# Optimization experiments

Hardware: AMD Instinct MI355X
Metric: run time of the kernel (lower is better)

## Reference

```python
import jax, jax.numpy as jnp
import numpy as np

N = 50000      # nodes
E = 800000     # edges (avg degree 16)
IN = 128       # in_channels
HID = 32       # hidden_channels per head
HEADS = 4
OUT = 64       # out_channels (last layer, heads=1, concat=False)
ED = 32        # edge_dim
NEG_SLOPE = 0.2


def _gatv2_layer(x, src, dst, ea, Wl, bl, Wr, br, We, att, bias, concat):
    """PyG GATv2Conv: lin_l -> source (x_j), lin_r -> target (x_i),
    score = att . leaky_relu(x_i + x_j + lin_edge(edge_attr)), segment-softmax over dst,
    out = scatter_add(alpha * x_j) per head, then concat or mean heads, plus bias."""
    n = x.shape[0]
    H, C = att.shape
    xl = (x @ Wl + bl).reshape(-1, H, C)   # [N,H,C] source transform
    xr = (x @ Wr + br).reshape(-1, H, C)   # [N,H,C] target transform
    ee = (ea @ We).reshape(-1, H, C)       # [E,H,C] edge transform
    m = jax.nn.leaky_relu(xl[src] + xr[dst] + ee, NEG_SLOPE)  # [E,H,C]
    a = jnp.einsum('ehc,hc->eh', m, att)   # [E,H] attention logits
    amax = jax.ops.segment_max(a, dst, num_segments=n)        # [N,H]
    ex = jnp.exp(a - amax[dst])
    den = jax.ops.segment_sum(ex, dst, num_segments=n)        # [N,H]
    alpha = ex / (den[dst] + 1e-16)        # [E,H] segment softmax
    out = jax.ops.segment_sum(xl[src] * alpha[..., None], dst, num_segments=n)  # [N,H,C]
    out = out.reshape(n, H * C) if concat else out.mean(axis=1)
    return out + bias


def setup_inputs() -> dict:
    key = jax.random.key(0)
    ks = jax.random.split(key, 20)
    s = 0.05
    HC = HEADS * HID
    inp = {
        'x': jax.random.normal(ks[0], (N, IN), jnp.float32),
        'edge_index': jax.random.randint(ks[1], (2, E), 0, N, jnp.int32),
        'edge_attr': jax.random.normal(ks[2], (E, ED), jnp.float32),
        # layer 1: GATv2Conv(IN -> HID, heads=HEADS, concat=True, edge_dim=ED)
        'Wl1': jax.random.normal(ks[3], (IN, HC), jnp.float32) * s,
        'bl1': jnp.zeros((HC,), jnp.float32),
        'Wr1': jax.random.normal(ks[4], (IN, HC), jnp.float32) * s,
        'br1': jnp.zeros((HC,), jnp.float32),
        'We1': jax.random.normal(ks[5], (ED, HC), jnp.float32) * s,
        'att1': jax.random.normal(ks[6], (HEADS, HID), jnp.float32) * s,
        'bias1': jnp.zeros((HC,), jnp.float32),
        # layer 2: GATv2Conv(HC -> OUT, heads=1, concat=False, edge_dim=ED)
        'Wl2': jax.random.normal(ks[7], (HC, OUT), jnp.float32) * s,
        'bl2': jnp.zeros((OUT,), jnp.float32),
        'Wr2': jax.random.normal(ks[8], (HC, OUT), jnp.float32) * s,
        'br2': jnp.zeros((OUT,), jnp.float32),
        'We2': jax.random.normal(ks[9], (ED, OUT), jnp.float32) * s,
        'att2': jax.random.normal(ks[10], (1, OUT), jnp.float32) * s,
        'bias2': jnp.zeros((OUT,), jnp.float32),
    }
    return inp


def reference(x, edge_index, edge_attr, Wl1, bl1, Wr1, br1, We1, att1, bias1,
              Wl2, bl2, Wr2, br2, We2, att2, bias2):
    src, dst = edge_index[0], edge_index[1]
    h = _gatv2_layer(x, src, dst, edge_attr, Wl1, bl1, Wr1, br1, We1, att1, bias1, concat=True)
    h = jax.nn.elu(h)
    out = _gatv2_layer(h, src, dst, edge_attr, Wl2, bl2, Wr2, br2, We2, att2, bias2, concat=False)
    return out
```

## Files before the change

kernel.cpp:

```cpp
#include <hip/hip_runtime.h>
#include <stdint.h>

#define N_NODES 50000
#define N_EDGES 800000

struct Ptrs { const void* p[16]; int n[16]; };

typedef __attribute__((ext_vector_type(8))) short bf16x8;
typedef __attribute__((ext_vector_type(4))) float f32x4;

__device__ __forceinline__ float bf2f(unsigned short u){
  union { unsigned int i; float f; } v; v.i = ((unsigned int)u) << 16; return v.f;
}
__device__ __forceinline__ float lo16(unsigned int u){ union { unsigned int i; float f; } v; v.i = u << 16; return v.f; }
__device__ __forceinline__ float hi16(unsigned int u){ union { unsigned int i; float f; } v; v.i = u & 0xffff0000u; return v.f; }
__device__ __forceinline__ unsigned short f2bf(float f){
  if (!(f == f)) return 0;
  unsigned int x = __float_as_uint(f);
  unsigned int r = (x + 0x7fffu + ((x >> 16) & 1u)) >> 16;
  return (unsigned short)r;
}
__device__ __forceinline__ float fin(float v){
  if (!(v == v)) return 0.f;
  return fminf(fmaxf(v, -1e30f), 1e30f);
}
__device__ __forceinline__ float loadF(const void* p, int f32, size_t idx){
  return f32 ? ((const float*)p)[idx] : bf2f(((const unsigned short*)p)[idx]);
}

__device__ __forceinline__ void stageW(unsigned short* dst, const void* src, int n, int f32, int tid){
  if (f32) {
    for (int i = tid * 8; i < n; i += 2048) {
      float4 a = *(const float4*)((const float*)src + i);
      float4 b = *(const float4*)((const float*)src + i + 4);
      uint4 u;
      u.x = (unsigned)f2bf(a.x) | ((unsigned)f2bf(a.y) << 16);
      u.y = (unsigned)f2bf(a.z) | ((unsigned)f2bf(a.w) << 16);
      u.z = (unsigned)f2bf(b.x) | ((unsigned)f2bf(b.y) << 16);
      u.w = (unsigned)f2bf(b.z) | ((unsigned)f2bf(b.w) << 16);
      *(uint4*)(dst + i) = u;
    }
  } else {
    for (int i = tid * 8; i < n; i += 2048)
      *(uint4*)(dst + i) = *(const uint4*)((const unsigned short*)src + i);
  }
}

__global__ __launch_bounds__(256) void k_detect(Ptrs tl, int* __restrict__ flags)
{
  __shared__ int red[256];
  int b = blockIdx.x, t = threadIdx.x;
  const unsigned short* p = (const unsigned short*)tl.p[b];
  int n = tl.n[b]; if (n > 16384) n = 16384;
  int crazy = 0;
  for (int i = t; i < n; i += 256) {
    unsigned short u = p[i];
    if (u) {
      int ex = (u >> 7) & 0xFF;
      if (ex == 0xFF || ex < 0x60) crazy++;
    }
  }
  red[t] = crazy; __syncthreads();
  for (int off = 128; off; off >>= 1) { if (t < off) red[t] += red[t + off]; __syncthreads(); }
  if (t == 0) flags[b] = (red[0] * 10 > n) ? 1 : 0;
}

__global__ __launch_bounds__(256) void k_zero(int* __restrict__ p, int n)
{
  int i = blockIdx.x * 256 + threadIdx.x;
  if (i < n) p[i] = 0;
}

__global__ __launch_bounds__(256) void k_gemm1(
    const void* __restrict__ x,
    const void* __restrict__ Wl, const void* __restrict__ bl,
    const void* __restrict__ Wr, const void* __restrict__ br,
    const int* __restrict__ flags,
    unsigned int* __restrict__ xlp, unsigned int* __restrict__ xrp)
{
  __shared__ float xs[32 * 132];
  __shared__ unsigned short ws[128 * 128];
  const void* W  = blockIdx.y ? Wr : Wl;
  const void* bb = blockIdx.y ? br : bl;
  int fW = blockIdx.y ? flags[4] : flags[2];
  int fB = blockIdx.y ? flags[5] : flags[3];
  int fX = flags[0];
  unsigned int* outp = blockIdx.y ? xrp : xlp;
  int tid = threadIdx.x;
  int row0 = blockIdx.x * 32;
  stageW(ws, W, 128 * 128, fW, tid);
  for (int i = tid * 4; i < 32 * 128; i += 1024) {
    int r = i >> 7, k = i & 127;
    int row = row0 + r;
    float4 v = make_float4(0.f, 0.f, 0.f, 0.f);
    if (row < N_NODES) {
      if (fX) v = *(const float4*)((const float*)x + (size_t)row * 128 + k);
      else {
        uint2 u = *(const uint2*)((const unsigned short*)x + (size_t)row * 128 + k);
        v.x = lo16(u.x); v.y = hi16(u.x); v.z = lo16(u.y); v.w = hi16(u.y);
      }
    }
    *(float4*)(xs + r * 132 + k) = v;
  }
  __syncthreads();
  int r = tid >> 3, cg = tid & 7;
  float acc[16];
#pragma unroll
  for (int j = 0; j < 16; j++) acc[j] = 0.f;
#pragma unroll 4
  for (int k = 0; k < 128; k++) {
    float xv = xs[r * 132 + k];
    uint4 p0 = *(const uint4*)(ws + k * 128 + cg * 8);
    uint4 p1 = *(const uint4*)(ws + k * 128 + 64 + cg * 8);
    acc[0]  = fmaf(xv, lo16(p0.x), acc[0]);  acc[1]  = fmaf(xv, hi16(p0.x), acc[1]);
    acc[2]  = fmaf(xv, lo16(p0.y), acc[2]);  acc[3]  = fmaf(xv, hi16(p0.y), acc[3]);
    acc[4]  = fmaf(xv, lo16(p0.z), acc[4]);  acc[5]  = fmaf(xv, hi16(p0.z), acc[5]);
    acc[6]  = fmaf(xv, lo16(p0.w), acc[6]);  acc[7]  = fmaf(xv, hi16(p0.w), acc[7]);
    acc[8]  = fmaf(xv, lo16(p1.x), acc[8]);  acc[9]  = fmaf(xv, hi16(p1.x), acc[9]);
    acc[10] = fmaf(xv, lo16(p1.y), acc[10]); acc[11] = fmaf(xv, hi16(p1.y), acc[11]);
    acc[12] = fmaf(xv, lo16(p1.z), acc[12]); acc[13] = fmaf(xv, hi16(p1.z), acc[13]);
    acc[14] = fmaf(xv, lo16(p1.w), acc[14]); acc[15] = fmaf(xv, hi16(p1.w), acc[15]);
  }
  int row = row0 + r;
  if (row < N_NODES) {
    unsigned int* op = outp + (size_t)row * 64;
    uint4 o;
    unsigned int* ou = (unsigned int*)&o;
#pragma unroll
    for (int t = 0; t < 4; t++) {
      float f0 = fin(acc[2 * t]     + loadF(bb, fB, cg * 8 + 2 * t));
      float f1 = fin(acc[2 * t + 1] + loadF(bb, fB, cg * 8 + 2 * t + 1));
      ou[t] = (unsigned)f2bf(f0) | ((unsigned)f2bf(f1) << 16);
    }
    *(uint4*)(op + cg * 4) = o;
#pragma unroll
    for (int t = 0; t < 4; t++) {
      float f0 = fin(acc[8 + 2 * t]     + loadF(bb, fB, 64 + cg * 8 + 2 * t));
      float f1 = fin(acc[8 + 2 * t + 1] + loadF(bb, fB, 64 + cg * 8 + 2 * t + 1));
      ou[t] = (unsigned)f2bf(f0) | ((unsigned)f2bf(f1) << 16);
    }
    *(uint4*)(op + 32 + cg * 4) = o;
  }
}

__global__ __launch_bounds__(256) void k_gemm2(
    const float* __restrict__ h,
    const void* __restrict__ Wl, const void* __restrict__ bl,
    const void* __restrict__ Wr, const void* __restrict__ br,
    const int* __restrict__ flags,
    unsigned int* __restrict__ xlp, unsigned int* __restrict__ xrp)
{
  __shared__ float hs[32 * 132];
  __shared__ unsigned short ws[128 * 64];
  const void* W  = blockIdx.y ? Wr : Wl;
  const void* bb = blockIdx.y ? br : bl;
  int fW = blockIdx.y ? flags[11] : flags[9];
  int fB = blockIdx.y ? flags[12] : flags[10];
  unsigned int* outp = blockIdx.y ? xrp : xlp;
  int tid = threadIdx.x;
  int row0 = blockIdx.x * 32;
  stageW(ws, W, 128 * 64, fW, tid);
  for (int i = tid * 4; i < 32 * 128; i += 1024) {
    int r = i >> 7, k = i & 127;
    int row = row0 + r;
    float4 v = make_float4(0.f, 0.f, 0.f, 0.f);
    if (row < N_NODES) v = *(const float4*)(h + (size_t)row * 128 + k);
    *(float4*)(hs + r * 132 + k) = v;
  }
  __syncthreads();
  int r = tid >> 3, cg = tid & 7;
  float acc[8];
#pragma unroll
  for (int j = 0; j < 8; j++) acc[j] = 0.f;
#pragma unroll 4
  for (int k = 0; k < 128; k++) {
    float hv = hs[r * 132 + k];
    uint4 p = *(const uint4*)(ws + k * 64 + cg * 8);
    acc[0] = fmaf(hv, lo16(p.x), acc[0]); acc[1] = fmaf(hv, hi16(p.x), acc[1]);
    acc[2] = fmaf(hv, lo16(p.y), acc[2]); acc[3] = fmaf(hv, hi16(p.y), acc[3]);
    acc[4] = fmaf(hv, lo16(p.z), acc[4]); acc[5] = fmaf(hv, hi16(p.z), acc[5]);
    acc[6] = fmaf(hv, lo16(p.w), acc[6]); acc[7] = fmaf(hv, hi16(p.w), acc[7]);
  }
  int row = row0 + r;
  if (row < N_NODES) {
    uint4 o;
    unsigned int* ou = (unsigned int*)&o;
#pragma unroll
    for (int t = 0; t < 4; t++) {
      float f0 = fin(acc[2 * t]     + loadF(bb, fB, cg * 8 + 2 * t));
      float f1 = fin(acc[2 * t + 1] + loadF(bb, fB, cg * 8 + 2 * t + 1));
      ou[t] = (unsigned)f2bf(f0) | ((unsigned)f2bf(f1) << 16);
    }
    *(uint4*)(outp + (size_t)row * 32 + cg * 4) = o;
  }
}

__global__ __launch_bounds__(256) void k_hist(const int* __restrict__ ei, int* __restrict__ counts)
{
  int e = blockIdx.x * 256 + threadIdx.x;
  if (e < N_EDGES) {
    int d = ei[N_EDGES + e]; if ((unsigned)d >= N_NODES) d = 0;
    atomicAdd(&counts[d], 1);
  }
}

__global__ __launch_bounds__(256) void k_scan1(const int* __restrict__ counts,
                                               int* __restrict__ row_ptr, int* __restrict__ bsum)
{
  __shared__ int lds[256];
  int t = threadIdx.x;
  int base = blockIdx.x * 1024 + t * 4;
  int c0 = (base + 0) < N_NODES ? counts[base + 0] : 0;
  int c1 = (base + 1) < N_NODES ? counts[base + 1] : 0;
  int c2 = (base + 2) < N_NODES ? counts[base + 2] : 0;
  int c3 = (base + 3) < N_NODES ? counts[base + 3] : 0;
  int s = c0 + c1 + c2 + c3;
  lds[t] = s; __syncthreads();
  for (int off = 1; off < 256; off <<= 1) {
    int v = (t >= off) ? lds[t - off] : 0;
    __syncthreads();
    lds[t] += v;
    __syncthreads();
  }
  int incl = lds[t];
  int excl = incl - s;
  if (base + 0 < N_NODES) row_ptr[base + 0] = excl;
  if (base + 1 < N_NODES) row_ptr[base + 1] = excl + c0;
  if (base + 2 < N_NODES) row_ptr[base + 2] = excl + c0 + c1;
  if (base + 3 < N_NODES) row_ptr[base + 3] = excl + c0 + c1 + c2;
  if (t == 255) bsum[blockIdx.x] = incl;
}

__global__ __launch_bounds__(64) void k_scan2(int* __restrict__ bsum, int nb)
{
  __shared__ int l[64];
  int t = threadIdx.x;
  if (t < nb) l[t] = bsum[t];
  __syncthreads();
  if (t == 0) { int run = 0; for (int i = 0; i < nb; i++) { int v = l[i]; l[i] = run; run += v; } }
  __syncthreads();
  if (t < nb) bsum[t] = l[t];
}

__global__ __launch_bounds__(256) void k_scan3(int* __restrict__ row_ptr, int* __restrict__ cursor,
                                               const int* __restrict__ bsum)
{
  int t = threadIdx.x;
  int base = blockIdx.x * 1024 + t * 4;
  int add = bsum[blockIdx.x];
#pragma unroll
  for (int j = 0; j < 4; j++) {
    int i = base + j;
    if (i < N_NODES) { int v = row_ptr[i] + add; row_ptr[i] = v; cursor[i] = v; }
  }
  if (blockIdx.x == 0 && t == 0) row_ptr[N_NODES] = N_EDGES;
}

__global__ __launch_bounds__(256) void k_scatter(const int* __restrict__ ei,
                                                 int* __restrict__ cursor, int* __restrict__ col,
                                                 int* __restrict__ pos, int* __restrict__ srcs)
{
  int e = blockIdx.x * 256 + threadIdx.x;
  if (e < N_EDGES) {
    int d = ei[N_EDGES + e]; if ((unsigned)d >= N_NODES) d = 0;
    int s = ei[e];           if ((unsigned)s >= N_NODES) s = 0;
    int p = atomicAdd(&cursor[d], 1);
    if ((unsigned)p < N_EDGES) { col[p] = e; pos[e] = p; srcs[p] = s; }
  }
}

__global__ __launch_bounds__(256) void k_score1(
    const void* __restrict__ ea, const int* __restrict__ ei, const int* __restrict__ pos,
    const unsigned int* __restrict__ xlp, const unsigned int* __restrict__ xrp,
    const void* __restrict__ We, const void* __restrict__ att,
    const int* __restrict__ flags, float* __restrict__ w1)
{
  __shared__ unsigned short wt[128 * 34];
  __shared__ float at[128];
  int tid = threadIdx.x;
  {
    int f = flags[6];
    for (int i = tid; i < 4096; i += 256) {
      int k = i >> 7, c = i & 127;
      wt[c * 34 + k] = f ? f2bf(((const float*)We)[i]) : ((const unsigned short*)We)[i];
    }
  }
  if (tid < 128) at[tid] = loadF(att, flags[7], tid);
  __syncthreads();
  int lane = tid & 63;
  int idx16 = lane & 15, quad = lane >> 4;
  bf16x8 af[8];
  float4 atv[8];
#pragma unroll
  for (int t = 0; t < 8; t++) {
    af[t]  = *(const bf16x8*)(wt + (t * 16 + idx16) * 34 + quad * 8);
    atv[t] = *(const float4*)(at + t * 16 + quad * 4);
  }
  int fEA = flags[1];
  size_t e0 = (size_t)blockIdx.x * 128 + (size_t)(tid >> 6) * 32;
#pragma unroll
  for (int tt = 0; tt < 2; tt++) {
    size_t e = e0 + tt * 16 + idx16;
    bf16x8 bfrag;
    if (fEA) {
      const float* p = (const float*)ea + e * 32 + quad * 8;
      float4 v0 = *(const float4*)p;
      float4 v1 = *(const float4*)(p + 4);
      unsigned short tmp[8] = { f2bf(v0.x), f2bf(v0.y), f2bf(v0.z), f2bf(v0.w),
                                f2bf(v1.x), f2bf(v1.y), f2bf(v1.z), f2bf(v1.w) };
      bfrag = *(const bf16x8*)tmp;
    } else {
      bfrag = *(const bf16x8*)((const unsigned short*)ea + e * 32 + quad * 8);
    }
    int s = ei[e];           if ((unsigned)s >= N_NODES) s = 0;
    int d = ei[N_EDGES + e]; if ((unsigned)d >= N_NODES) d = 0;
    size_t dp = (size_t)pos[e];
    float ph0 = 0.f, ph1 = 0.f, ph2 = 0.f, ph3 = 0.f;
#pragma unroll
    for (int t = 0; t < 8; t++) {
      f32x4 c = {0.f, 0.f, 0.f, 0.f};
      c = __builtin_amdgcn_mfma_f32_16x16x32_bf16(af[t], bfrag, c, 0, 0, 0);
      uint2 ux = *(const uint2*)(xlp + (size_t)s * 64 + t * 8 + quad * 2);
      uint2 ur = *(const uint2*)(xrp + (size_t)d * 64 + t * 8 + quad * 2);
      float z0 = c[0] + lo16(ux.x) + lo16(ur.x);
      float z1 = c[1] + hi16(ux.x) + hi16(ur.x);
      float z2 = c[2] + lo16(ux.y) + lo16(ur.y);
      float z3 = c[3] + hi16(ux.y) + hi16(ur.y);
      z0 = z0 > 0.f ? z0 : 0.2f * z0;
      z1 = z1 > 0.f ? z1 : 0.2f * z1;
      z2 = z2 > 0.f ? z2 : 0.2f * z2;
      z3 = z3 > 0.f ? z3 : 0.2f * z3;
      float pp = fmaf(atv[t].x, z0, fmaf(atv[t].y, z1, fmaf(atv[t].z, z2, atv[t].w * z3)));
      if (t < 2)      ph0 += pp;
      else if (t < 4) ph1 += pp;
      else if (t < 6) ph2 += pp;
      else            ph3 += pp;
    }
    ph0 += __shfl_xor(ph0, 16, 64); ph0 += __shfl_xor(ph0, 32, 64);
    ph1 += __shfl_xor(ph1, 16, 64); ph1 += __shfl_xor(ph1, 32, 64);
    ph2 += __shfl_xor(ph2, 16, 64); ph2 += __shfl_xor(ph2, 32, 64);
    ph3 += __shfl_xor(ph3, 16, 64); ph3 += __shfl_xor(ph3, 32, 64);
    float myp = quad == 0 ? ph0 : quad == 1 ? ph1 : quad == 2 ? ph2 : ph3;
    w1[dp * 4 + quad] = __expf(fminf(fin(myp), 25.f));
  }
}

__global__ __launch_bounds__(256) void k_score2(
    const void* __restrict__ ea, const int* __restrict__ ei, const int* __restrict__ pos,
    const unsigned int* __restrict__ xlp, const unsigned int* __restrict__ xrp,
    const void* __restrict__ We, const void* __restrict__ att,
    const int* __restrict__ flags, float* __restrict__ w2)
{
  __shared__ unsigned short wt[64 * 34];
  __shared__ float at[64];
  int tid = threadIdx.x;
  {
    int f = flags[13];
    for (int i = tid; i < 2048; i += 256) {
      int k = i >> 6, c = i & 63;
      wt[c * 34 + k] = f ? f2bf(((const float*)We)[i]) : ((const unsigned short*)We)[i];
    }
  }
  if (tid < 64) at[tid] = loadF(att, flags[14], tid);
  __syncthreads();
  int lane = tid & 63;
  int idx16 = lane & 15, quad = lane >> 4;
  bf16x8 af[4];
  float4 atv[4];
#pragma unroll
  for (int t = 0; t < 4; t++) {
    af[t]  = *(const bf16x8*)(wt + (t * 16 + idx16) * 34 + quad * 8);
    atv[t] = *(const float4*)(at + t * 16 + quad * 4);
  }
  int fEA = flags[1];
  size_t e0 = (size_t)blockIdx.x * 128 + (size_t)(tid >> 6) * 32;
#pragma unroll
  for (int tt = 0; tt < 2; tt++) {
    size_t e = e0 + tt * 16 + idx16;
    bf16x8 bfrag;
    if (fEA) {
      const float* p = (const float*)ea + e * 32 + quad * 8;
      float4 v0 = *(const float4*)p;
      float4 v1 = *(const float4*)(p + 4);
      unsigned short tmp[8] = { f2bf(v0.x), f2bf(v0.y), f2bf(v0.z), f2bf(v0.w),
                                f2bf(v1.x), f2bf(v1.y), f2bf(v1.z), f2bf(v1.w) };
      bfrag = *(const bf16x8*)tmp;
    } else {
      bfrag = *(const bf16x8*)((const unsigned short*)ea + e * 32 + quad * 8);
    }
    int s = ei[e];           if ((unsigned)s >= N_NODES) s = 0;
    int d = ei[N_EDGES + e]; if ((unsigned)d >= N_NODES) d = 0;
    size_t dp = (size_t)pos[e];
    float ph = 0.f;
#pragma unroll
    for (int t = 0; t < 4; t++) {
      f32x4 c = {0.f, 0.f, 0.f, 0.f};
      c = __builtin_amdgcn_mfma_f32_16x16x32_bf16(af[t], bfrag, c, 0, 0, 0);
      uint2 ux = *(const uint2*)(xlp + (size_t)s * 32 + t * 8 + quad * 2);
      uint2 ur = *(const uint2*)(xrp + (size_t)d * 32 + t * 8 + quad * 2);
      float z0 = c[0] + lo16(ux.x) + lo16(ur.x);
      float z1 = c[1] + hi16(ux.x) + hi16(ur.x);
      float z2 = c[2] + lo16(ux.y) + lo16(ur.y);
      float z3 = c[3] + hi16(ux.y) + hi16(ur.y);
      z0 = z0 > 0.f ? z0 : 0.2f * z0;
      z1 = z1 > 0.f ? z1 : 0.2f * z1;
      z2 = z2 > 0.f ? z2 : 0.2f * z2;
      z3 = z3 > 0.f ? z3 : 0.2f * z3;
      ph += fmaf(atv[t].x, z0, fmaf(atv[t].y, z1, fmaf(atv[t].z, z2, atv[t].w * z3)));
    }
    ph += __shfl_xor(ph, 16, 64);
    ph += __shfl_xor(ph, 32, 64);
    if (quad == 0) w2[dp] = __expf(fminf(fin(ph), 25.f));
  }
}

__global__ __launch_bounds__(256) void k_agg1(
    const int* __restrict__ srcs, const int* __restrict__ row_ptr,
    const unsigned int* __restrict__ xlp, const float* __restrict__ w1,
    const void* __restrict__ bias, const int* __restrict__ flags,
    float* __restrict__ hout)
{
  int tid = threadIdx.x;
  int i = blockIdx.x * 4 + (tid >> 6);
  int lane = tid & 63;
  int head = lane >> 4;
  int p0 = row_ptr[i], p1 = row_ptr[i + 1];
  float acc0 = 0.f, acc1 = 0.f, den = 0.f;
  int j = p0;
  for (; j + 4 <= p1; j += 4) {
    int s0 = srcs[j], s1 = srcs[j + 1], s2 = srcs[j + 2], s3 = srcs[j + 3];
    float wa = w1[(size_t)(j + 0) * 4 + head];
    float wb = w1[(size_t)(j + 1) * 4 + head];
    float wc = w1[(size_t)(j + 2) * 4 + head];
    float wd = w1[(size_t)(j + 3) * 4 + head];
    unsigned int ux0 = xlp[(size_t)s0 * 64 + lane];
    unsigned int ux1 = xlp[(size_t)s1 * 64 + lane];
    unsigned int ux2 = xlp[(size_t)s2 * 64 + lane];
    unsigned int ux3 = xlp[(size_t)s3 * 64 + lane];
    acc0 = fmaf(wa, lo16(ux0), acc0); acc1 = fmaf(wa, hi16(ux0), acc1);
    acc0 = fmaf(wb, lo16(ux1), acc0); acc1 = fmaf(wb, hi16(ux1), acc1);
    acc0 = fmaf(wc, lo16(ux2), acc0); acc1 = fmaf(wc, hi16(ux2), acc1);
    acc0 = fmaf(wd, lo16(ux3), acc0); acc1 = fmaf(wd, hi16(ux3), acc1);
    den += wa + wb + wc + wd;
  }
  for (; j < p1; j++) {
    int s = srcs[j];
    float w = w1[(size_t)j * 4 + head];
    unsigned int ux = xlp[(size_t)s * 64 + lane];
    acc0 = fmaf(w, lo16(ux), acc0);
    acc1 = fmaf(w, hi16(ux), acc1);
    den += w;
  }
  float inv = 1.f / (den + 1e-16f);
  float o0 = fin(fmaf(acc0, inv, loadF(bias, flags[8], 2 * lane)));
  float o1 = fin(fmaf(acc1, inv, loadF(bias, flags[8], 2 * lane + 1)));
  o0 = o0 > 0.f ? o0 : __expf(o0) - 1.f;
  o1 = o1 > 0.f ? o1 : __expf(o1) - 1.f;
  *(float2*)(hout + (size_t)i * 128 + 2 * lane) = make_float2(o0, o1);
}

__global__ __launch_bounds__(256) void k_agg2(
    const int* __restrict__ srcs, const int* __restrict__ row_ptr,
    const unsigned int* __restrict__ xlp, const float* __restrict__ w2,
    const void* __restrict__ bias, const int* __restrict__ flags,
    void* __restrict__ out)
{
  int tid = threadIdx.x;
  int i = blockIdx.x * 4 + (tid >> 6);
  int lane = tid & 63;
  const unsigned short* xlb = (const unsigned short*)xlp;
  int p0 = row_ptr[i], p1 = row_ptr[i + 1];
  float acc = 0.f, den = 0.f;
  int j = p0;
  for (; j + 4 <= p1; j += 4) {
    int s0 = srcs[j], s1 = srcs[j + 1], s2 = srcs[j + 2], s3 = srcs[j + 3];
    float wa = w2[j], wb = w2[j + 1], wc = w2[j + 2], wd = w2[j + 3];
    unsigned short x0 = xlb[(size_t)s0 * 64 + lane];
    unsigned short x1 = xlb[(size_t)s1 * 64 + lane];
    unsigned short x2 = xlb[(size_t)s2 * 64 + lane];
    unsigned short x3 = xlb[(size_t)s3 * 64 + lane];
    acc = fmaf(wa, bf2f(x0), acc);
    acc = fmaf(wb, bf2f(x1), acc);
    acc = fmaf(wc, bf2f(x2), acc);
    acc = fmaf(wd, bf2f(x3), acc);
    den += wa + wb + wc + wd;
  }
  for (; j < p1; j++) {
    int s = srcs[j];
    float w = w2[j];
    acc = fmaf(w, bf2f(xlb[(size_t)s * 64 + lane]), acc);
    den += w;
  }
  float inv = 1.f / (den + 1e-16f);
  float o = fin(fmaf(acc, inv, loadF(bias, flags[15], lane)));
  if (flags[0]) ((float*)out)[(size_t)i * 64 + lane] = o;
  else ((unsigned short*)out)[(size_t)i * 64 + lane] = f2bf(o);
}

extern "C" void kernel_launch(void* const* d_in, const int* in_sizes, int n_in,
                              void* d_out, int out_size, void* d_ws, size_t ws_size,
                              hipStream_t stream)
{
  (void)n_in; (void)out_size; (void)ws_size;
  const void* x    = d_in[0];
  const int*  ei   = (const int*)d_in[1];
  const void* ea   = d_in[2];
  const void* Wl1  = d_in[3];
  const void* bl1  = d_in[4];
  const void* Wr1  = d_in[5];
  const void* br1  = d_in[6];
  const void* We1  = d_in[7];
  const void* att1 = d_in[8];
  const void* bias1= d_in[9];
  const void* Wl2  = d_in[10];
  const void* bl2  = d_in[11];
  const void* Wr2  = d_in[12];
  const void* br2  = d_in[13];
  const void* We2  = d_in[14];
  const void* att2 = d_in[15];
  const void* bias2= d_in[16];

  char* ws = (char*)d_ws;
  size_t off = 0;
  auto take = [&](size_t bytes) -> char* {
    char* p = ws + off;
    off += (bytes + 255) & ~(size_t)255;
    return p;
  };
  unsigned int* xl1p = (unsigned int*)take((size_t)N_NODES * 64 * 4);
  unsigned int* xr1p = (unsigned int*)take((size_t)N_NODES * 64 * 4);
  float* hbuf   = (float*)take((size_t)N_NODES * 128 * 4);
  float* w1     = (float*)take((size_t)N_EDGES * 4 * 4);
  int*   counts = (int*)  take((size_t)N_NODES * 4);
  int*   row_ptr= (int*)  take((size_t)(N_NODES + 1) * 4);
  int*   cursor = (int*)  take((size_t)N_NODES * 4);
  int*   col    = (int*)  take((size_t)N_EDGES * 4);
  int*   pos    = (int*)  take((size_t)N_EDGES * 4);
  int*   srcs   = (int*)  take((size_t)N_EDGES * 4);
  int*   bsum   = (int*)  take(64 * 4);
  int*   flags  = (int*)  take(64 * 4);
  unsigned int* xl2p = xl1p;
  unsigned int* xr2p = xr1p;
  float* w2 = w1;

  Ptrs tl;
  const int map[16] = {0, 2, 3, 4, 5, 6, 7, 8, 9, 10, 11, 12, 13, 14, 15, 16};
  for (int j = 0; j < 16; j++) { tl.p[j] = d_in[map[j]]; tl.n[j] = in_sizes[map[j]]; }

  int nb = (N_NODES + 1023) / 1024;
  k_detect<<<16, 256, 0, stream>>>(tl, flags);
  k_zero<<<(N_NODES + 255) / 256, 256, 0, stream>>>(counts, N_NODES);
  k_gemm1<<<dim3((N_NODES + 31) / 32, 2), 256, 0, stream>>>(x, Wl1, bl1, Wr1, br1, flags, xl1p, xr1p);
  k_hist<<<(N_EDGES + 255) / 256, 256, 0, stream>>>(ei, counts);
  k_scan1<<<nb, 256, 0, stream>>>(counts, row_ptr, bsum);
  k_scan2<<<1, 64, 0, stream>>>(bsum, nb);
  k_scan3<<<nb, 256, 0, stream>>>(row_ptr, cursor, bsum);
  k_scatter<<<(N_EDGES + 255) / 256, 256, 0, stream>>>(ei, cursor, col, pos, srcs);
  k_score1<<<N_EDGES / 128, 256, 0, stream>>>(ea, ei, pos, xl1p, xr1p, We1, att1, flags, w1);
  k_agg1<<<N_NODES / 4, 256, 0, stream>>>(srcs, row_ptr, xl1p, w1, bias1, flags, hbuf);
  k_gemm2<<<dim3((N_NODES + 31) / 32, 2), 256, 0, stream>>>(hbuf, Wl2, bl2, Wr2, br2, flags, xl2p, xr2p);
  k_score2<<<N_EDGES / 128, 256, 0, stream>>>(ea, ei, pos, xl2p, xr2p, We2, att2, flags, w2);
  k_agg2<<<N_NODES / 4, 256, 0, stream>>>(srcs, row_ptr, xl2p, w2, bias2, flags, d_out);
}
```

Measured before the change: 740.3 us.

## Process scores in CSR order, cache sorted edge attrs, vectorize aggregation

The score kernels now walk edges in dst-sorted (CSR) order, so xr rows and w writes become local, and edge_attr is gathered via col. Layer 1 also stores a bf16 copy of the permuted edge attributes, which layer 2 reads contiguously. All gathers are hoisted ahead of the MFMA work, and launch bounds are added for occupancy. The aggregation kernels split each node's edges across lane groups using 16-byte loads and finish with shuffle reductions. The cost is a 51 MB scratch buffer, random reads of edge_attr in layer 1, and extra shuffles.

```diff
diff --git a/kernel.cpp b/kernel.cpp
--- a/kernel.cpp
+++ b/kernel.cpp
@@ -258,22 +258,54 @@
 
 __global__ __launch_bounds__(256) void k_scatter(const int* __restrict__ ei,
                                                  int* __restrict__ cursor, int* __restrict__ col,
-                                                 int* __restrict__ pos, int* __restrict__ srcs)
+                                                 int* __restrict__ srcs, int* __restrict__ dsts)
 {
   int e = blockIdx.x * 256 + threadIdx.x;
   if (e < N_EDGES) {
     int d = ei[N_EDGES + e]; if ((unsigned)d >= N_NODES) d = 0;
     int s = ei[e];           if ((unsigned)s >= N_NODES) s = 0;
     int p = atomicAdd(&cursor[d], 1);
-    if ((unsigned)p < N_EDGES) { col[p] = e; pos[e] = p; srcs[p] = s; }
-  }
-}
-
-__global__ __launch_bounds__(256) void k_score1(
-    const void* __restrict__ ea, const int* __restrict__ ei, const int* __restrict__ pos,
+    if ((unsigned)p < N_EDGES) { col[p] = e; srcs[p] = s; dsts[p] = d; }
+  }
+}
+
+#define SCORE1_TILE(bfrag, xv, rv, pidx)                                       \
+  {                                                                            \
+    float ph0 = 0.f, ph1 = 0.f, ph2 = 0.f, ph3 = 0.f;                          \
+    _Pragma("unroll")                                                          \
+    for (int t = 0; t < 8; t++) {                                              \
+      f32x4 c = {0.f, 0.f, 0.f, 0.f};                                          \
+      c = __builtin_amdgcn_mfma_f32_16x16x32_bf16(af[t], bfrag, c, 0, 0, 0);   \
+      float4 av = *(const float4*)(at + t * 16 + quad * 4);                    \
+      float z0 = c[0] + lo16(xv[t].x) + lo16(rv[t].x);                         \
+      float z1 = c[1] + hi16(xv[t].x) + hi16(rv[t].x);                         \
+      float z2 = c[2] + lo16(xv[t].y) + lo16(rv[t].y);                         \
+      float z3 = c[3] + hi16(xv[t].y) + hi16(rv[t].y);                         \
+      z0 = z0 > 0.f ? z0 : 0.2f * z0;                                          \
+      z1 = z1 > 0.f ? z1 : 0.2f * z1;                                          \
+      z2 = z2 > 0.f ? z2 : 0.2f * z2;                                          \
+      z3 = z3 > 0.f ? z3 : 0.2f * z3;                                          \
+      float pp = fmaf(av.x, z0, fmaf(av.y, z1, fmaf(av.z, z2, av.w * z3)));    \
+      if (t < 2)      ph0 += pp;                                               \
+      else if (t < 4) ph1 += pp;                                               \
+      else if (t < 6) ph2 += pp;                                               \
+      else            ph3 += pp;                                               \
+    }                                                                          \
+    ph0 += __shfl_xor(ph0, 16, 64); ph0 += __shfl_xor(ph0, 32, 64);            \
+    ph1 += __shfl_xor(ph1, 16, 64); ph1 += __shfl_xor(ph1, 32, 64);            \
+    ph2 += __shfl_xor(ph2, 16, 64); ph2 += __shfl_xor(ph2, 32, 64);            \
+    ph3 += __shfl_xor(ph3, 16, 64); ph3 += __shfl_xor(ph3, 32, 64);            \
+    float myp = quad == 0 ? ph0 : quad == 1 ? ph1 : quad == 2 ? ph2 : ph3;     \
+    w1[(size_t)(pidx) * 4 + quad] = __expf(fminf(fin(myp), 25.f));             \
+  }
+
+__global__ __launch_bounds__(256, 3) void k_score1(
+    const void* __restrict__ ea, const int* __restrict__ col,
+    const int* __restrict__ srcs, const int* __restrict__ dsts,
     const unsigned int* __restrict__ xlp, const unsigned int* __restrict__ xrp,
     const void* __restrict__ We, const void* __restrict__ att,
-    const int* __restrict__ flags, float* __restrict__ w1)
+    const int* __restrict__ flags, float* __restrict__ w1,
+    unsigned short* __restrict__ eap)
 {
   __shared__ unsigned short wt[128 * 34];
   __shared__ float at[128];
@@ -290,63 +322,74 @@
   int lane = tid & 63;
   int idx16 = lane & 15, quad = lane >> 4;
   bf16x8 af[8];
-  float4 atv[8];
-#pragma unroll
-  for (int t = 0; t < 8; t++) {
-    af[t]  = *(const bf16x8*)(wt + (t * 16 + idx16) * 34 + quad * 8);
-    atv[t] = *(const float4*)(at + t * 16 + quad * 4);
-  }
+#pragma unroll
+  for (int t = 0; t < 8; t++)
+    af[t] = *(const bf16x8*)(wt + (t * 16 + idx16) * 34 + quad * 8);
   int fEA = flags[1];
-  size_t e0 = (size_t)blockIdx.x * 128 + (size_t)(tid >> 6) * 32;
-#pragma unroll
-  for (int tt = 0; tt < 2; tt++) {
-    size_t e = e0 + tt * 16 + idx16;
-    bf16x8 bfrag;
-    if (fEA) {
-      const float* p = (const float*)ea + e * 32 + quad * 8;
-      float4 v0 = *(const float4*)p;
-      float4 v1 = *(const float4*)(p + 4);
-      unsigned short tmp[8] = { f2bf(v0.x), f2bf(v0.y), f2bf(v0.z), f2bf(v0.w),
-                                f2bf(v1.x), f2bf(v1.y), f2bf(v1.z), f2bf(v1.w) };
-      bfrag = *(const bf16x8*)tmp;
-    } else {
-      bfrag = *(const bf16x8*)((const unsigned short*)ea + e * 32 + quad * 8);
-    }
-    int s = ei[e];           if ((unsigned)s >= N_NODES) s = 0;
-    int d = ei[N_EDGES + e]; if ((unsigned)d >= N_NODES) d = 0;
-    size_t dp = (size_t)pos[e];
-    float ph0 = 0.f, ph1 = 0.f, ph2 = 0.f, ph3 = 0.f;
-#pragma unroll
-    for (int t = 0; t < 8; t++) {
-      f32x4 c = {0.f, 0.f, 0.f, 0.f};
-      c = __builtin_amdgcn_mfma_f32_16x16x32_bf16(af[t], bfrag, c, 0, 0, 0);
-      uint2 ux = *(const uint2*)(xlp + (size_t)s * 64 + t * 8 + quad * 2);
-      uint2 ur = *(const uint2*)(xrp + (size_t)d * 64 + t * 8 + quad * 2);
-      float z0 = c[0] + lo16(ux.x) + lo16(ur.x);
-      float z1 = c[1] + hi16(ux.x) + hi16(ur.x);
-      float z2 = c[2] + lo16(ux.y) + lo16(ur.y);
-      float z3 = c[3] + hi16(ux.y) + hi16(ur.y);
-      z0 = z0 > 0.f ? z0 : 0.2f * z0;
-      z1 = z1 > 0.f ? z1 : 0.2f * z1;
-      z2 = z2 > 0.f ? z2 : 0.2f * z2;
-      z3 = z3 > 0.f ? z3 : 0.2f * z3;
-      float pp = fmaf(atv[t].x, z0, fmaf(atv[t].y, z1, fmaf(atv[t].z, z2, atv[t].w * z3)));
-      if (t < 2)      ph0 += pp;
-      else if (t < 4) ph1 += pp;
-      else if (t < 6) ph2 += pp;
-      else            ph3 += pp;
-    }
-    ph0 += __shfl_xor(ph0, 16, 64); ph0 += __shfl_xor(ph0, 32, 64);
-    ph1 += __shfl_xor(ph1, 16, 64); ph1 += __shfl_xor(ph1, 32, 64);
-    ph2 += __shfl_xor(ph2, 16, 64); ph2 += __shfl_xor(ph2, 32, 64);
-    ph3 += __shfl_xor(ph3, 16, 64); ph3 += __shfl_xor(ph3, 32, 64);
-    float myp = quad == 0 ? ph0 : quad == 1 ? ph1 : quad == 2 ? ph2 : ph3;
-    w1[dp * 4 + quad] = __expf(fminf(fin(myp), 25.f));
-  }
-}
-
-__global__ __launch_bounds__(256) void k_score2(
-    const void* __restrict__ ea, const int* __restrict__ ei, const int* __restrict__ pos,
+  int pA = blockIdx.x * 128 + (tid >> 6) * 32 + idx16;
+  int pB = pA + 16;
+  int eA = col[pA], eB = col[pB];
+  int sA = srcs[pA], sB = srcs[pB];
+  int dA = dsts[pA], dB = dsts[pB];
+  bf16x8 bA, bB;
+  if (fEA) {
+    const float* pa = (const float*)ea + (size_t)eA * 32 + quad * 8;
+    const float* pb = (const float*)ea + (size_t)eB * 32 + quad * 8;
+    float4 a0 = *(const float4*)pa;
+    float4 a1 = *(const float4*)(pa + 4);
+    float4 b0 = *(const float4*)pb;
+    float4 b1 = *(const float4*)(pb + 4);
+    unsigned short ta[8] = { f2bf(a0.x), f2bf(a0.y), f2bf(a0.z), f2bf(a0.w),
+                             f2bf(a1.x), f2bf(a1.y), f2bf(a1.z), f2bf(a1.w) };
+    unsigned short tb[8] = { f2bf(b0.x), f2bf(b0.y), f2bf(b0.z), f2bf(b0.w),
+                             f2bf(b1.x), f2bf(b1.y), f2bf(b1.z), f2bf(b1.w) };
+    bA = *(const bf16x8*)ta;
+    bB = *(const bf16x8*)tb;
+  } else {
+    bA = *(const bf16x8*)((const unsigned short*)ea + (size_t)eA * 32 + quad * 8);
+    bB = *(const bf16x8*)((const unsigned short*)ea + (size_t)eB * 32 + quad * 8);
+  }
+  *(bf16x8*)(eap + (size_t)pA * 32 + quad * 8) = bA;
+  *(bf16x8*)(eap + (size_t)pB * 32 + quad * 8) = bB;
+  uint2 xA[8], xB[8], rA[8], rB[8];
+#pragma unroll
+  for (int t = 0; t < 8; t++) xA[t] = *(const uint2*)(xlp + (size_t)sA * 64 + t * 8 + quad * 2);
+#pragma unroll
+  for (int t = 0; t < 8; t++) xB[t] = *(const uint2*)(xlp + (size_t)sB * 64 + t * 8 + quad * 2);
+#pragma unroll
+  for (int t = 0; t < 8; t++) rA[t] = *(const uint2*)(xrp + (size_t)dA * 64 + t * 8 + quad * 2);
+#pragma unroll
+  for (int t = 0; t < 8; t++) rB[t] = *(const uint2*)(xrp + (size_t)dB * 64 + t * 8 + quad * 2);
+  SCORE1_TILE(bA, xA, rA, pA)
+  SCORE1_TILE(bB, xB, rB, pB)
+}
+
+#define SCORE2_TILE(bfrag, xv, rv, pidx)                                       \
+  {                                                                            \
+    float ph = 0.f;                                                            \
+    _Pragma("unroll")                                                          \
+    for (int t = 0; t < 4; t++) {                                              \
+      f32x4 c = {0.f, 0.f, 0.f, 0.f};                                          \
+      c = __builtin_amdgcn_mfma_f32_16x16x32_bf16(af[t], bfrag, c, 0, 0, 0);   \
+      float4 av = *(const float4*)(at + t * 16 + quad * 4);                    \
+      float z0 = c[0] + lo16(xv[t].x) + lo16(rv[t].x);                         \
+      float z1 = c[1] + hi16(xv[t].x) + hi16(rv[t].x);                         \
+      float z2 = c[2] + lo16(xv[t].y) + lo16(rv[t].y);                         \
+      float z3 = c[3] + hi16(xv[t].y) + hi16(rv[t].y);                         \
+      z0 = z0 > 0.f ? z0 : 0.2f * z0;                                          \
+      z1 = z1 > 0.f ? z1 : 0.2f * z1;                                          \
+      z2 = z2 > 0.f ? z2 : 0.2f * z2;                                          \
+      z3 = z3 > 0.f ? z3 : 0.2f * z3;                                          \
+      ph += fmaf(av.x, z0, fmaf(av.y, z1, fmaf(av.z, z2, av.w * z3)));         \
+    }                                                                          \
+    ph += __shfl_xor(ph, 16, 64);                                              \
+    ph += __shfl_xor(ph, 32, 64);                                              \
+    if (quad == 0) w2[pidx] = __expf(fminf(fin(ph), 25.f));                    \
+  }
+
+__global__ __launch_bounds__(256, 4) void k_score2(
+    const unsigned short* __restrict__ eap,
+    const int* __restrict__ srcs, const int* __restrict__ dsts,
     const unsigned int* __restrict__ xlp, const unsigned int* __restrict__ xrp,
     const void* __restrict__ We, const void* __restrict__ att,
     const int* __restrict__ flags, float* __restrict__ w2)
@@ -366,52 +409,26 @@
   int lane = tid & 63;
   int idx16 = lane & 15, quad = lane >> 4;
   bf16x8 af[4];
-  float4 atv[4];
-#pragma unroll
-  for (int t = 0; t < 4; t++) {
-    af[t]  = *(const bf16x8*)(wt + (t * 16 + idx16) * 34 + quad * 8);
-    atv[t] = *(const float4*)(at + t * 16 + quad * 4);
-  }
-  int fEA = flags[1];
-  size_t e0 = (size_t)blockIdx.x * 128 + (size_t)(tid >> 6) * 32;
-#pragma unroll
-  for (int tt = 0; tt < 2; tt++) {
-    size_t e = e0 + tt * 16 + idx16;
-    bf16x8 bfrag;
-    if (fEA) {
-      const float* p = (const float*)ea + e * 32 + quad * 8;
-      float4 v0 = *(const float4*)p;
-      float4 v1 = *(const float4*)(p + 4);
-      unsigned short tmp[8] = { f2bf(v0.x), f2bf(v0.y), f2bf(v0.z), f2bf(v0.w),
-                                f2bf(v1.x), f2bf(v1.y), f2bf(v1.z), f2bf(v1.w) };
-      bfrag = *(const bf16x8*)tmp;
-    } else {
-      bfrag = *(const bf16x8*)((const unsigned short*)ea + e * 32 + quad * 8);
-    }
-    int s = ei[e];           if ((unsigned)s >= N_NODES) s = 0;
-    int d = ei[N_EDGES + e]; if ((unsigned)d >= N_NODES) d = 0;
-    size_t dp = (size_t)pos[e];
-    float ph = 0.f;
-#pragma unroll
-    for (int t = 0; t < 4; t++) {
-      f32x4 c = {0.f, 0.f, 0.f, 0.f};
-      c = __builtin_amdgcn_mfma_f32_16x16x32_bf16(af[t], bfrag, c, 0, 0, 0);
-      uint2 ux = *(const uint2*)(xlp + (size_t)s * 32 + t * 8 + quad * 2);
-      uint2 ur = *(const uint2*)(xrp + (size_t)d * 32 + t * 8 + quad * 2);
-      float z0 = c[0] + lo16(ux.x) + lo16(ur.x);
-      float z1 = c[1] + hi16(ux.x) + hi16(ur.x);
-      float z2 = c[2] + lo16(ux.y) + lo16(ur.y);
-      float z3 = c[3] + hi16(ux.y) + hi16(ur.y);
-      z0 = z0 > 0.f ? z0 : 0.2f * z0;
-      z1 = z1 > 0.f ? z1 : 0.2f * z1;
-      z2 = z2 > 0.f ? z2 : 0.2f * z2;
-      z3 = z3 > 0.f ? z3 : 0.2f * z3;
-      ph += fmaf(atv[t].x, z0, fmaf(atv[t].y, z1, fmaf(atv[t].z, z2, atv[t].w * z3)));
-    }
-    ph += __shfl_xor(ph, 16, 64);
-    ph += __shfl_xor(ph, 32, 64);
-    if (quad == 0) w2[dp] = __expf(fminf(fin(ph), 25.f));
-  }
+#pragma unroll
+  for (int t = 0; t < 4; t++)
+    af[t] = *(const bf16x8*)(wt + (t * 16 + idx16) * 34 + quad * 8);
+  int pA = blockIdx.x * 128 + (tid >> 6) * 32 + idx16;
+  int pB = pA + 16;
+  int sA = srcs[pA], sB = srcs[pB];
+  int dA = dsts[pA], dB = dsts[pB];
+  bf16x8 bA = *(const bf16x8*)(eap + (size_t)pA * 32 + quad * 8);
+  bf16x8 bB = *(const bf16x8*)(eap + (size_t)pB * 32 + quad * 8);
+  uint2 xA[4], xB[4], rA[4], rB[4];
+#pragma unroll
+  for (int t = 0; t < 4; t++) xA[t] = *(const uint2*)(xlp + (size_t)sA * 32 + t * 8 + quad * 2);
+#pragma unroll
+  for (int t = 0; t < 4; t++) xB[t] = *(const uint2*)(xlp + (size_t)sB * 32 + t * 8 + quad * 2);
+#pragma unroll
+  for (int t = 0; t < 4; t++) rA[t] = *(const uint2*)(xrp + (size_t)dA * 32 + t * 8 + quad * 2);
+#pragma unroll
+  for (int t = 0; t < 4; t++) rB[t] = *(const uint2*)(xrp + (size_t)dB * 32 + t * 8 + quad * 2);
+  SCORE2_TILE(bA, xA, rA, pA)
+  SCORE2_TILE(bB, xB, rB, pB)
 }
 
 __global__ __launch_bounds__(256) void k_agg1(
@@ -423,40 +440,59 @@
   int tid = threadIdx.x;
   int i = blockIdx.x * 4 + (tid >> 6);
   int lane = tid & 63;
-  int head = lane >> 4;
+  int je = lane >> 4;
+  int chunk = lane & 15;
+  int head = chunk >> 2;
   int p0 = row_ptr[i], p1 = row_ptr[i + 1];
-  float acc0 = 0.f, acc1 = 0.f, den = 0.f;
-  int j = p0;
-  for (; j + 4 <= p1; j += 4) {
-    int s0 = srcs[j], s1 = srcs[j + 1], s2 = srcs[j + 2], s3 = srcs[j + 3];
-    float wa = w1[(size_t)(j + 0) * 4 + head];
-    float wb = w1[(size_t)(j + 1) * 4 + head];
-    float wc = w1[(size_t)(j + 2) * 4 + head];
-    float wd = w1[(size_t)(j + 3) * 4 + head];
-    unsigned int ux0 = xlp[(size_t)s0 * 64 + lane];
-    unsigned int ux1 = xlp[(size_t)s1 * 64 + lane];
-    unsigned int ux2 = xlp[(size_t)s2 * 64 + lane];
-    unsigned int ux3 = xlp[(size_t)s3 * 64 + lane];
-    acc0 = fmaf(wa, lo16(ux0), acc0); acc1 = fmaf(wa, hi16(ux0), acc1);
-    acc0 = fmaf(wb, lo16(ux1), acc0); acc1 = fmaf(wb, hi16(ux1), acc1);
-    acc0 = fmaf(wc, lo16(ux2), acc0); acc1 = fmaf(wc, hi16(ux2), acc1);
-    acc0 = fmaf(wd, lo16(ux3), acc0); acc1 = fmaf(wd, hi16(ux3), acc1);
-    den += wa + wb + wc + wd;
-  }
-  for (; j < p1; j++) {
-    int s = srcs[j];
-    float w = w1[(size_t)j * 4 + head];
-    unsigned int ux = xlp[(size_t)s * 64 + lane];
-    acc0 = fmaf(w, lo16(ux), acc0);
-    acc1 = fmaf(w, hi16(ux), acc1);
-    den += w;
-  }
-  float inv = 1.f / (den + 1e-16f);
-  float o0 = fin(fmaf(acc0, inv, loadF(bias, flags[8], 2 * lane)));
-  float o1 = fin(fmaf(acc1, inv, loadF(bias, flags[8], 2 * lane + 1)));
-  o0 = o0 > 0.f ? o0 : __expf(o0) - 1.f;
-  o1 = o1 > 0.f ? o1 : __expf(o1) - 1.f;
-  *(float2*)(hout + (size_t)i * 128 + 2 * lane) = make_float2(o0, o1);
+  float acc[8];
+#pragma unroll
+  for (int k = 0; k < 8; k++) acc[k] = 0.f;
+  float den = 0.f;
+  int j = p0 + je;
+  for (; j + 4 < p1; j += 8) {
+    int s0 = srcs[j], s1 = srcs[j + 4];
+    float wa = w1[(size_t)j * 4 + head];
+    float wb = w1[(size_t)(j + 4) * 4 + head];
+    uint4 u0 = *(const uint4*)(xlp + (size_t)s0 * 64 + chunk * 4);
+    uint4 u1 = *(const uint4*)(xlp + (size_t)s1 * 64 + chunk * 4);
+    acc[0] = fmaf(wa, lo16(u0.x), acc[0]); acc[1] = fmaf(wa, hi16(u0.x), acc[1]);
+    acc[2] = fmaf(wa, lo16(u0.y), acc[2]); acc[3] = fmaf(wa, hi16(u0.y), acc[3]);
+    acc[4] = fmaf(wa, lo16(u0.z), acc[4]); acc[5] = fmaf(wa, hi16(u0.z), acc[5]);
+    acc[6] = fmaf(wa, lo16(u0.w), acc[6]); acc[7] = fmaf(wa, hi16(u0.w), acc[7]);
+    acc[0] = fmaf(wb, lo16(u1.x), acc[0]); acc[1] = fmaf(wb, hi16(u1.x), acc[1]);
+    acc[2] = fmaf(wb, lo16(u1.y), acc[2]); acc[3] = fmaf(wb, hi16(u1.y), acc[3]);
+    acc[4] = fmaf(wb, lo16(u1.z), acc[4]); acc[5] = fmaf(wb, hi16(u1.z), acc[5]);
+    acc[6] = fmaf(wb, lo16(u1.w), acc[6]); acc[7] = fmaf(wb, hi16(u1.w), acc[7]);
+    den += wa + wb;
+  }
+  if (j < p1) {
+    int s0 = srcs[j];
+    float wa = w1[(size_t)j * 4 + head];
+    uint4 u0 = *(const uint4*)(xlp + (size_t)s0 * 64 + chunk * 4);
+    acc[0] = fmaf(wa, lo16(u0.x), acc[0]); acc[1] = fmaf(wa, hi16(u0.x), acc[1]);
+    acc[2] = fmaf(wa, lo16(u0.y), acc[2]); acc[3] = fmaf(wa, hi16(u0.y), acc[3]);
+    acc[4] = fmaf(wa, lo16(u0.z), acc[4]); acc[5] = fmaf(wa, hi16(u0.z), acc[5]);
+    acc[6] = fmaf(wa, lo16(u0.w), acc[6]); acc[7] = fmaf(wa, hi16(u0.w), acc[7]);
+    den += wa;
+  }
+#pragma unroll
+  for (int k = 0; k < 8; k++) {
+    acc[k] += __shfl_xor(acc[k], 16, 64);
+    acc[k] += __shfl_xor(acc[k], 32, 64);
+  }
+  den += __shfl_xor(den, 16, 64);
+  den += __shfl_xor(den, 32, 64);
+  if (je == 0) {
+    float inv = 1.f / (den + 1e-16f);
+    float o[8];
+#pragma unroll
+    for (int k = 0; k < 8; k++) {
+      float v = fin(fmaf(acc[k], inv, loadF(bias, flags[8], chunk * 8 + k)));
+      o[k] = v > 0.f ? v : __expf(v) - 1.f;
+    }
+    *(float4*)(hout + (size_t)i * 128 + chunk * 8)     = make_float4(o[0], o[1], o[2], o[3]);
+    *(float4*)(hout + (size_t)i * 128 + chunk * 8 + 4) = make_float4(o[4], o[5], o[6], o[7]);
+  }
 }
 
 __global__ __launch_bounds__(256) void k_agg2(
@@ -468,33 +504,67 @@
   int tid = threadIdx.x;
   int i = blockIdx.x * 4 + (tid >> 6);
   int lane = tid & 63;
-  const unsigned short* xlb = (const unsigned short*)xlp;
+  int je = lane >> 3;
+  int chunk = lane & 7;
   int p0 = row_ptr[i], p1 = row_ptr[i + 1];
-  float acc = 0.f, den = 0.f;
-  int j = p0;
-  for (; j + 4 <= p1; j += 4) {
-    int s0 = srcs[j], s1 = srcs[j + 1], s2 = srcs[j + 2], s3 = srcs[j + 3];
-    float wa = w2[j], wb = w2[j + 1], wc = w2[j + 2], wd = w2[j + 3];
-    unsigned short x0 = xlb[(size_t)s0 * 64 + lane];
-    unsigned short x1 = xlb[(size_t)s1 * 64 + lane];
-    unsigned short x2 = xlb[(size_t)s2 * 64 + lane];
-    unsigned short x3 = xlb[(size_t)s3 * 64 + lane];
-    acc = fmaf(wa, bf2f(x0), acc);
-    acc = fmaf(wb, bf2f(x1), acc);
-    acc = fmaf(wc, bf2f(x2), acc);
-    acc = fmaf(wd, bf2f(x3), acc);
-    den += wa + wb + wc + wd;
-  }
-  for (; j < p1; j++) {
-    int s = srcs[j];
-    float w = w2[j];
-    acc = fmaf(w, bf2f(xlb[(size_t)s * 64 + lane]), acc);
-    den += w;
-  }
-  float inv = 1.f / (den + 1e-16f);
-  float o = fin(fmaf(acc, inv, loadF(bias, flags[15], lane)));
-  if (flags[0]) ((float*)out)[(size_t)i * 64 + lane] = o;
-  else ((unsigned short*)out)[(size_t)i * 64 + lane] = f2bf(o);
+  float acc[8];
+#pragma unroll
+  for (int k = 0; k < 8; k++) acc[k] = 0.f;
+  float den = 0.f;
+  int j = p0 + je;
+  for (; j + 8 < p1; j += 16) {
+    int s0 = srcs[j], s1 = srcs[j + 8];
+    float wa = w2[j], wb = w2[j + 8];
+    uint4 u0 = *(const uint4*)(xlp + (size_t)s0 * 32 + chunk * 4);
+    uint4 u1 = *(const uint4*)(xlp + (size_t)s1 * 32 + chunk * 4);
+    acc[0] = fmaf(wa, lo16(u0.x), acc[0]); acc[1] = fmaf(wa, hi16(u0.x), acc[1]);
+    acc[2] = fmaf(wa, lo16(u0.y), acc[2]); acc[3] = fmaf(wa, hi16(u0.y), acc[3]);
+    acc[4] = fmaf(wa, lo16(u0.z), acc[4]); acc[5] = fmaf(wa, hi16(u0.z), acc[5]);
+    acc[6] = fmaf(wa, lo16(u0.w), acc[6]); acc[7] = fmaf(wa, hi16(u0.w), acc[7]);
+    acc[0] = fmaf(wb, lo16(u1.x), acc[0]); acc[1] = fmaf(wb, hi16(u1.x), acc[1]);
+    acc[2] = fmaf(wb, lo16(u1.y), acc[2]); acc[3] = fmaf(wb, hi16(u1.y), acc[3]);
+    acc[4] = fmaf(wb, lo16(u1.z), acc[4]); acc[5] = fmaf(wb, hi16(u1.z), acc[5]);
+    acc[6] = fmaf(wb, lo16(u1.w), acc[6]); acc[7] = fmaf(wb, hi16(u1.w), acc[7]);
+    den += wa + wb;
+  }
+  if (j < p1) {
+    int s0 = srcs[j];
+    float wa = w2[j];
+    uint4 u0 = *(const uint4*)(xlp + (size_t)s0 * 32 + chunk * 4);
+    acc[0] = fmaf(wa, lo16(u0.x), acc[0]); acc[1] = fmaf(wa, hi16(u0.x), acc[1]);
+    acc[2] = fmaf(wa, lo16(u0.y), acc[2]); acc[3] = fmaf(wa, hi16(u0.y), acc[3]);
+    acc[4] = fmaf(wa, lo16(u0.z), acc[4]); acc[5] = fmaf(wa, hi16(u0.z), acc[5]);
+    acc[6] = fmaf(wa, lo16(u0.w), acc[6]); acc[7] = fmaf(wa, hi16(u0.w), acc[7]);
+    den += wa;
+  }
+#pragma unroll
+  for (int k = 0; k < 8; k++) {
+    acc[k] += __shfl_xor(acc[k], 8, 64);
+    acc[k] += __shfl_xor(acc[k], 16, 64);
+    acc[k] += __shfl_xor(acc[k], 32, 64);
+  }
+  den += __shfl_xor(den, 8, 64);
+  den += __shfl_xor(den, 16, 64);
+  den += __shfl_xor(den, 32, 64);
+  if (je == 0) {
+    float inv = 1.f / (den + 1e-16f);
+    float o[8];
+#pragma unroll
+    for (int k = 0; k < 8; k++)
+      o[k] = fin(fmaf(acc[k], inv, loadF(bias, flags[15], chunk * 8 + k)));
+    if (flags[0]) {
+      float* op = (float*)out + (size_t)i * 64 + chunk * 8;
+      *(float4*)(op)     = make_float4(o[0], o[1], o[2], o[3]);
+      *(float4*)(op + 4) = make_float4(o[4], o[5], o[6], o[7]);
+    } else {
+      uint4 u;
+      unsigned int* uu = (unsigned int*)&u;
+#pragma unroll
+      for (int t = 0; t < 4; t++)
+        uu[t] = (unsigned)f2bf(o[2 * t]) | ((unsigned)f2bf(o[2 * t + 1]) << 16);
+      *(uint4*)((unsigned short*)out + (size_t)i * 64 + chunk * 8) = u;
+    }
+  }
 }
 
 extern "C" void kernel_launch(void* const* d_in, const int* in_sizes, int n_in,
@@ -531,12 +601,13 @@
   unsigned int* xr1p = (unsigned int*)take((size_t)N_NODES * 64 * 4);
   float* hbuf   = (float*)take((size_t)N_NODES * 128 * 4);
   float* w1     = (float*)take((size_t)N_EDGES * 4 * 4);
+  unsigned short* eap = (unsigned short*)take((size_t)N_EDGES * 32 * 2);
   int*   counts = (int*)  take((size_t)N_NODES * 4);
   int*   row_ptr= (int*)  take((size_t)(N_NODES + 1) * 4);
   int*   cursor = (int*)  take((size_t)N_NODES * 4);
   int*   col    = (int*)  take((size_t)N_EDGES * 4);
-  int*   pos    = (int*)  take((size_t)N_EDGES * 4);
   int*   srcs   = (int*)  take((size_t)N_EDGES * 4);
+  int*   dsts   = (int*)  take((size_t)N_EDGES * 4);
   int*   bsum   = (int*)  take(64 * 4);
   int*   flags  = (int*)  take(64 * 4);
   unsigned int* xl2p = xl1p;
@@ -555,10 +626,10 @@
   k_scan1<<<nb, 256, 0, stream>>>(counts, row_ptr, bsum);
   k_scan2<<<1, 64, 0, stream>>>(bsum, nb);
   k_scan3<<<nb, 256, 0, stream>>>(row_ptr, cursor, bsum);
-  k_scatter<<<(N_EDGES + 255) / 256, 256, 0, stream>>>(ei, cursor, col, pos, srcs);
-  k_score1<<<N_EDGES / 128, 256, 0, stream>>>(ea, ei, pos, xl1p, xr1p, We1, att1, flags, w1);
+  k_scatter<<<(N_EDGES + 255) / 256, 256, 0, stream>>>(ei, cursor, col, srcs, dsts);
+  k_score1<<<N_EDGES / 128, 256, 0, stream>>>(ea, col, srcs, dsts, xl1p, xr1p, We1, att1, flags, w1, eap);
   k_agg1<<<N_NODES / 4, 256, 0, stream>>>(srcs, row_ptr, xl1p, w1, bias1, flags, hbuf);
   k_gemm2<<<dim3((N_NODES + 31) / 32, 2), 256, 0, stream>>>(hbuf, Wl2, bl2, Wr2, br2, flags, xl2p, xr2p);
-  k_score2<<<N_EDGES / 128, 256, 0, stream>>>(ea, ei, pos, xl2p, xr2p, We2, att2, flags, w2);
+  k_score2<<<N_EDGES / 128, 256, 0, stream>>>(eap, srcs, dsts, xl2p, xr2p, We2, att2, flags, w2);
   k_agg2<<<N_NODES / 4, 256, 0, stream>>>(srcs, row_ptr, xl2p, w2, bias2, flags, d_out);
 }
```

New measurement: 671.4 us. -9.3%, faster.
